# Optimization experiments

Hardware: AMD Instinct MI355X
Metric: run time of the kernel (lower is better)

Reference implementation:

```python
import jax, jax.numpy as jnp
import numpy as np
import math

B, S, D, H, W = 4, 8192, 1024, 16, 512  # batch, seq, d_model, heads, attention_window
HD = D // H


def setup_inputs() -> dict:
    key = jax.random.key(0)
    ks = jax.random.split(key, 5)
    scale = 0.02
    return {
        "x": jax.random.normal(ks[0], (B, S, D), dtype=jnp.float32),
        "wq": jax.random.normal(ks[1], (D, D), dtype=jnp.float32) * scale,
        "bq": jnp.zeros((D,), dtype=jnp.float32),
        "wk": jax.random.normal(ks[2], (D, D), dtype=jnp.float32) * scale,
        "bk": jnp.zeros((D,), dtype=jnp.float32),
        "wv": jax.random.normal(ks[3], (D, D), dtype=jnp.float32) * scale,
        "bv": jnp.zeros((D,), dtype=jnp.float32),
        "wo": jax.random.normal(ks[4], (D, D), dtype=jnp.float32) * scale,
        "bo": jnp.zeros((D,), dtype=jnp.float32),
    }


def reference(x, wq, bq, wk, bk, wv, bv, wo, bo):
    # torch Linear: y = x @ W.T + b
    q = (x @ wq.T + bq).reshape(B, S, H, HD)
    k = (x @ wk.T + bk).reshape(B, S, H, HD)
    v = (x @ wv.T + bv).reshape(B, S, H, HD)

    nb = S // W  # number of query blocks
    qb = q.reshape(B, nb, W, H, HD)

    # pad keys/values by W at the front so every block sees a 2W key window
    kp = jnp.pad(k, ((0, 0), (W, 0), (0, 0), (0, 0)))
    vp = jnp.pad(v, ((0, 0), (W, 0), (0, 0), (0, 0)))
    # padded key indices for block n: [n*W, n*W + 2W) <-> original [n*W - W, n*W + W)
    idx = jnp.arange(nb)[:, None] * W + jnp.arange(2 * W)[None, :]  # [nb, 2W]
    kb = kp[:, idx]  # [B, nb, 2W, H, HD]
    vb = vp[:, idx]  # [B, nb, 2W, H, HD]

    scores = jnp.einsum('bnqhd,bnkhd->bnhqk', qb, kb) / math.sqrt(HD)
    valid = (idx >= W)  # padded (out-of-range) keys only occur for block 0
    scores = jnp.where(valid[None, :, None, None, :], scores, -jnp.inf)
    attn = jax.nn.softmax(scores, axis=-1)  # softmax over the block's key window

    out = jnp.einsum('bnhqk,bnkhd->bnqhd', attn, vb).reshape(B, S, D)
    return out @ wo.T + bo
```

## Files before the change

kernel.cpp:

```cpp
#include <hip/hip_runtime.h>
#include <hip/hip_bf16.h>
#include <cstdint>

typedef __bf16 bf16;
typedef __attribute__((ext_vector_type(8))) __bf16 bf16x8;
typedef __attribute__((ext_vector_type(4))) __bf16 bf16x4;
typedef __attribute__((ext_vector_type(4))) float f32x4;
typedef __attribute__((ext_vector_type(4))) unsigned int u32x4;

#define B_ 4
#define S_ 8192
#define D_ 1024
#define H_ 16
#define HD_ 64
#define W_ 512
#define M_ (B_*S_)

#define EXP2F(x) __builtin_amdgcn_exp2f(x)
#define MFMA16(a,b,c) __builtin_amdgcn_mfma_f32_16x16x32_bf16(a,b,c,0,0,0)

__device__ __forceinline__ void async16(const void* g, void* l) {
  __builtin_amdgcn_global_load_lds(
      (const __attribute__((address_space(1))) unsigned int*)g,
      (__attribute__((address_space(3))) unsigned int*)l, 16, 0, 0);
}

__global__ void cast_f32_bf16(const float* __restrict__ in, bf16* __restrict__ out, int n4) {
  int i = blockIdx.x * blockDim.x + threadIdx.x;
  int stride = gridDim.x * blockDim.x;
  for (; i < n4; i += stride) {
    f32x4 v = ((const f32x4*)in)[i];
    bf16x4 o = { (bf16)v[0], (bf16)v[1], (bf16)v[2], (bf16)v[3] };
    ((bf16x4*)out)[i] = o;
  }
}

template<int MODE>
__global__ void __launch_bounds__(256, 2) gemm_bt(
    const bf16* __restrict__ A, const bf16* __restrict__ Bw,
    const float* __restrict__ bias, void* __restrict__ outp, float scale)
{
  constexpr int K = D_, N = D_;
  __shared__ bf16 As[128*32];
  __shared__ bf16 Bs[128*32];
  int bid = blockIdx.x;
  int nid = (bid & 7) * 256 + (bid >> 3);
  int bm = nid >> 3, bn = nid & 7;
  const int tid = threadIdx.x, lane = tid & 63;
  const int w = tid >> 6, wr = w >> 1, wc = w & 1;
  f32x4 acc[4][4] = {};
  const int r0 = tid >> 2;
  const int kbyte = (tid & 3) * 16;
  const char* Ab = (const char*)(A + (size_t)bm * 128 * K);
  const char* Bb = (const char*)(Bw + (size_t)bn * 128 * K);
  for (int kt = 0; kt < K; kt += 32) {
    __syncthreads();
    const size_t cb = (size_t)kt * 2 + kbyte;
    async16(Ab + (size_t)r0      * (K*2) + cb, (char*)As + tid*16);
    async16(Ab + (size_t)(r0+64) * (K*2) + cb, (char*)As + 4096 + tid*16);
    async16(Bb + (size_t)r0      * (K*2) + cb, (char*)Bs + tid*16);
    async16(Bb + (size_t)(r0+64) * (K*2) + cb, (char*)Bs + 4096 + tid*16);
    __syncthreads();
    bf16x8 a[4], b[4];
#pragma unroll
    for (int mi = 0; mi < 4; ++mi)
      a[mi] = *(const bf16x8*)(As + (wr*64 + mi*16 + (lane & 15))*32 + ((lane >> 4)*8));
#pragma unroll
    for (int ni = 0; ni < 4; ++ni)
      b[ni] = *(const bf16x8*)(Bs + (wc*64 + ni*16 + (lane & 15))*32 + ((lane >> 4)*8));
#pragma unroll
    for (int mi = 0; mi < 4; ++mi)
#pragma unroll
      for (int ni = 0; ni < 4; ++ni)
        acc[mi][ni] = MFMA16(a[mi], b[ni], acc[mi][ni]);
  }
  int row0 = bm*128 + wr*64, col0 = bn*128 + wc*64;
  int rsub = (lane >> 4) * 4;
#pragma unroll
  for (int ni = 0; ni < 4; ++ni) {
    int col = col0 + ni*16 + (lane & 15);
    float bz = bias[col];
#pragma unroll
    for (int mi = 0; mi < 4; ++mi) {
#pragma unroll
      for (int r = 0; r < 4; ++r) {
        int row = row0 + mi*16 + rsub + r;
        float v = (acc[mi][ni][r] + bz) * scale;
        if (MODE == 0) {
          ((bf16*)outp)[(size_t)row * N + col] = (bf16)v;
        } else if (MODE == 1) {
          ((bf16*)outp)[((size_t)(row >> 13) * D_ + col) * S_ + (row & (S_-1))] = (bf16)v;
        } else {
          ((float*)outp)[(size_t)row * N + col] = v;
        }
      }
    }
  }
}

__global__ void __launch_bounds__(256, 3) attn_kernel(
    const bf16* __restrict__ Q, const bf16* __restrict__ Kb,
    const bf16* __restrict__ Vt, bf16* __restrict__ Ao)
{
  __shared__ char Klds[2][8192];
  __shared__ char Vlds[2][8192];
  __shared__ char Plds[4][2048];
  int x = blockIdx.x;
  int xcd = x & 7, qt = (x >> 3) & 7, gg = x >> 6;
  int g = xcd + 8 * gg;
  int h = g & 15, n = (g >> 4) & 15, b = g >> 8;
  int tid = threadIdx.x, lane = tid & 63, w = tid >> 6;
  int g4 = lane >> 4, qi = lane & 15;
  int qrow = n * W_ + qt * 64 + w * 16;

  const size_t qoff = ((size_t)(b * S_ + qrow + qi)) * D_ + h * 64 + g4 * 8;
  bf16x8 qf0 = *(const bf16x8*)(Q + qoff);
  bf16x8 qf1 = *(const bf16x8*)(Q + qoff + 32);

  const bf16* Kg = Kb + ((size_t)b * S_) * D_ + h * 64;
  const bf16* Vg = Vt + ((size_t)(b * H_ + h) * HD_) * S_;

  const int srow = tid >> 3, scol = tid & 7;
  const int sswz = (srow & 7) << 4;

  f32x4 o[4] = {};
  float m_r = -3.0e38f, l_r = 0.f;
  const int fsw = (qi & 7) << 4;
  char* pb = &Plds[w][0];

  const int c0 = (n == 0) ? 8 : 0;
  const int ksbase = (n - 1) * W_;

  u32x4 pk0, pk1, pv0, pv1;
  {
    int ks = ksbase + c0 * 64;
    pk0 = *(const u32x4*)(Kg + (size_t)(ks + srow)      * D_ + scol * 8);
    pk1 = *(const u32x4*)(Kg + (size_t)(ks + srow + 32) * D_ + scol * 8);
    pv0 = *(const u32x4*)(Vg + (size_t)srow        * S_ + ks + scol * 8);
    pv1 = *(const u32x4*)(Vg + (size_t)(srow + 32) * S_ + ks + scol * 8);
    *(u32x4*)(Klds[0] + srow        * 128 + ((scol * 16) ^ sswz)) = pk0;
    *(u32x4*)(Klds[0] + (srow + 32) * 128 + ((scol * 16) ^ sswz)) = pk1;
    *(u32x4*)(Vlds[0] + srow        * 128 + ((scol * 16) ^ sswz)) = pv0;
    *(u32x4*)(Vlds[0] + (srow + 32) * 128 + ((scol * 16) ^ sswz)) = pv1;
  }
  __syncthreads();
  int cur = 0;
  for (int c = c0; c < 16; ++c) {
    bool pre = (c < 15);
    if (pre) {
      int ks2 = ksbase + (c + 1) * 64;
      pk0 = *(const u32x4*)(Kg + (size_t)(ks2 + srow)      * D_ + scol * 8);
      pk1 = *(const u32x4*)(Kg + (size_t)(ks2 + srow + 32) * D_ + scol * 8);
      pv0 = *(const u32x4*)(Vg + (size_t)srow        * S_ + ks2 + scol * 8);
      pv1 = *(const u32x4*)(Vg + (size_t)(srow + 32) * S_ + ks2 + scol * 8);
    }
    const char* kbuf = Klds[cur];
    const char* vbuf = Vlds[cur];
    f32x4 st[4];
    __builtin_amdgcn_s_setprio(1);
#pragma unroll
    for (int ni = 0; ni < 4; ++ni) {
      const char* kbase = kbuf + (ni * 16 + qi) * 128;
      bf16x8 kf0 = *(const bf16x8*)(kbase + ((g4 * 16) ^ fsw));
      bf16x8 kf1 = *(const bf16x8*)(kbase + ((64 + g4 * 16) ^ fsw));
      f32x4 z = {};
      z = MFMA16(kf0, qf0, z);
      z = MFMA16(kf1, qf1, z);
      st[ni] = z;
    }
    __builtin_amdgcn_s_setprio(0);
    float mx = st[0][0];
#pragma unroll
    for (int ni = 0; ni < 4; ++ni)
#pragma unroll
      for (int r = 0; r < 4; ++r) mx = fmaxf(mx, st[ni][r]);
    mx = fmaxf(mx, __shfl_xor(mx, 16));
    mx = fmaxf(mx, __shfl_xor(mx, 32));
    if (!__all(mx - m_r <= 8.0f)) {
      float mn = fmaxf(m_r, mx);
      float sc = EXP2F(m_r - mn);
      m_r = mn;
      l_r *= sc;
#pragma unroll
      for (int ai = 0; ai < 4; ++ai)
#pragma unroll
        for (int r = 0; r < 4; ++r) o[ai][r] *= sc;
    }
    float ls = 0.f;
    bf16x4 pw[4];
#pragma unroll
    for (int ni = 0; ni < 4; ++ni)
#pragma unroll
      for (int r = 0; r < 4; ++r) {
        float p = EXP2F(st[ni][r] - m_r);
        ls += p;
        pw[ni][r] = (bf16)p;
      }
    l_r += ls;
#pragma unroll
    for (int ni = 0; ni < 4; ++ni)
      *(bf16x4*)(pb + qi * 128 + ((ni * 32 + g4 * 8) ^ fsw)) = pw[ni];
    asm volatile("s_waitcnt lgkmcnt(0)" ::: "memory");
    __builtin_amdgcn_sched_barrier(0);
    bf16x8 pa0 = *(const bf16x8*)(pb + qi * 128 + ((g4 * 16) ^ fsw));
    bf16x8 pa1 = *(const bf16x8*)(pb + qi * 128 + ((64 + g4 * 16) ^ fsw));
    __builtin_amdgcn_sched_barrier(0x7F);
    __builtin_amdgcn_s_setprio(1);
#pragma unroll
    for (int ai = 0; ai < 4; ++ai) {
      const char* vbase = vbuf + (ai * 16 + qi) * 128;
      bf16x8 vf0 = *(const bf16x8*)(vbase + ((g4 * 16) ^ fsw));
      bf16x8 vf1 = *(const bf16x8*)(vbase + ((64 + g4 * 16) ^ fsw));
      o[ai] = MFMA16(vf0, pa0, o[ai]);
      o[ai] = MFMA16(vf1, pa1, o[ai]);
    }
    __builtin_amdgcn_s_setprio(0);
    if (pre) {
      int nb = cur ^ 1;
      *(u32x4*)(Klds[nb] + srow        * 128 + ((scol * 16) ^ sswz)) = pk0;
      *(u32x4*)(Klds[nb] + (srow + 32) * 128 + ((scol * 16) ^ sswz)) = pk1;
      *(u32x4*)(Vlds[nb] + srow        * 128 + ((scol * 16) ^ sswz)) = pv0;
      *(u32x4*)(Vlds[nb] + (srow + 32) * 128 + ((scol * 16) ^ sswz)) = pv1;
    }
    __syncthreads();
    cur ^= 1;
  }
  float lt = l_r + __shfl_xor(l_r, 16);
  lt += __shfl_xor(lt, 32);
  float inv = 1.0f / lt;
  size_t orow = ((size_t)(b * S_ + qrow + qi)) * D_ + h * 64 + g4 * 4;
#pragma unroll
  for (int ai = 0; ai < 4; ++ai) {
    bf16x4 ov;
#pragma unroll
    for (int r = 0; r < 4; ++r) ov[r] = (bf16)(o[ai][r] * inv);
    *(bf16x4*)(Ao + orow + ai * 16) = ov;
  }
}

extern "C" void kernel_launch(void* const* d_in, const int* in_sizes, int n_in,
                              void* d_out, int out_size, void* d_ws, size_t ws_size,
                              hipStream_t stream) {
  const float* x  = (const float*)d_in[0];
  const float* wq = (const float*)d_in[1];
  const float* bq = (const float*)d_in[2];
  const float* wk = (const float*)d_in[3];
  const float* bk = (const float*)d_in[4];
  const float* wv = (const float*)d_in[5];
  const float* bv = (const float*)d_in[6];
  const float* wo = (const float*)d_in[7];
  const float* bo = (const float*)d_in[8];
  float* out = (float*)d_out;

  char* ws = (char*)d_ws;
  const size_t sz = (size_t)M_ * D_ * 2;
  bf16* xb  = (bf16*)(ws + 0*sz);
  bf16* qb  = (bf16*)(ws + 1*sz);
  bf16* kb  = (bf16*)(ws + 2*sz);
  bf16* vt  = (bf16*)(ws + 3*sz);
  bf16* ao  = (bf16*)(ws + 4*sz);
  bf16* wqb = (bf16*)(ws + 5*sz);
  bf16* wkb = wqb + (size_t)D_*D_;
  bf16* wvb = wkb + (size_t)D_*D_;
  bf16* wob = wvb + (size_t)D_*D_;

  cast_f32_bf16<<<2048, 256, 0, stream>>>(x,  xb,  M_*D_/4);
  cast_f32_bf16<<<512,  256, 0, stream>>>(wq, wqb, D_*D_/4);
  cast_f32_bf16<<<512,  256, 0, stream>>>(wk, wkb, D_*D_/4);
  cast_f32_bf16<<<512,  256, 0, stream>>>(wv, wvb, D_*D_/4);
  cast_f32_bf16<<<512,  256, 0, stream>>>(wo, wob, D_*D_/4);

  gemm_bt<0><<<2048, 256, 0, stream>>>(xb, wqb, bq, qb, 0.125f * 1.44269504f);
  gemm_bt<0><<<2048, 256, 0, stream>>>(xb, wkb, bk, kb, 1.0f);
  gemm_bt<1><<<2048, 256, 0, stream>>>(xb, wvb, bv, vt, 1.0f);

  attn_kernel<<<8192, 256, 0, stream>>>(qb, kb, vt, ao);

  gemm_bt<2><<<2048, 256, 0, stream>>>(ao, wob, bo, out, 1.0f);
}
```

Baseline: 614.5 us.

## Use 32x32 MFMA register-resident P in attention and double-buffer GEMM LDS

The attention kernel moves from 16x16x32 to 32x32x16 MFMA tiles, with each wave handling 32 query rows, so the grid is halved. The P matrix is repacked in registers using cvt_pk_bf16 and permlane32_swap instead of a round-trip through LDS. Separately, the projection GEMM double-buffers its LDS tiles with async loads and explicit vmcnt waits so global loads overlap the MFMAs. The risks are higher register pressure in attention and correctness of the hand-written lane permutation and waitcnt sequencing.

```diff
diff --git a/kernel.cpp b/kernel.cpp
--- a/kernel.cpp
+++ b/kernel.cpp
@@ -6,6 +6,7 @@
 typedef __attribute__((ext_vector_type(8))) __bf16 bf16x8;
 typedef __attribute__((ext_vector_type(4))) __bf16 bf16x4;
 typedef __attribute__((ext_vector_type(4))) float f32x4;
+typedef __attribute__((ext_vector_type(16))) float f32x16;
 typedef __attribute__((ext_vector_type(4))) unsigned int u32x4;
 
 #define B_ 4
@@ -18,6 +19,7 @@
 
 #define EXP2F(x) __builtin_amdgcn_exp2f(x)
 #define MFMA16(a,b,c) __builtin_amdgcn_mfma_f32_16x16x32_bf16(a,b,c,0,0,0)
+#define MFMA32(a,b,c) __builtin_amdgcn_mfma_f32_32x32x16_bf16(a,b,c,0,0,0)
 
 __device__ __forceinline__ void async16(const void* g, void* l) {
   __builtin_amdgcn_global_load_lds(
@@ -41,8 +43,8 @@
     const float* __restrict__ bias, void* __restrict__ outp, float scale)
 {
   constexpr int K = D_, N = D_;
-  __shared__ bf16 As[128*32];
-  __shared__ bf16 Bs[128*32];
+  __shared__ bf16 As[2][128*32];
+  __shared__ bf16 Bs[2][128*32];
   int bid = blockIdx.x;
   int nid = (bid & 7) * 256 + (bid >> 3);
   int bm = nid >> 3, bn = nid & 7;
@@ -53,26 +55,38 @@
   const int kbyte = (tid & 3) * 16;
   const char* Ab = (const char*)(A + (size_t)bm * 128 * K);
   const char* Bb = (const char*)(Bw + (size_t)bn * 128 * K);
-  for (int kt = 0; kt < K; kt += 32) {
-    __syncthreads();
+
+  auto stage = [&](int kt, int buf) {
     const size_t cb = (size_t)kt * 2 + kbyte;
-    async16(Ab + (size_t)r0      * (K*2) + cb, (char*)As + tid*16);
-    async16(Ab + (size_t)(r0+64) * (K*2) + cb, (char*)As + 4096 + tid*16);
-    async16(Bb + (size_t)r0      * (K*2) + cb, (char*)Bs + tid*16);
-    async16(Bb + (size_t)(r0+64) * (K*2) + cb, (char*)Bs + 4096 + tid*16);
-    __syncthreads();
+    async16(Ab + (size_t)r0      * (K*2) + cb, (char*)&As[buf][0] + tid*16);
+    async16(Ab + (size_t)(r0+64) * (K*2) + cb, (char*)&As[buf][0] + 4096 + tid*16);
+    async16(Bb + (size_t)r0      * (K*2) + cb, (char*)&Bs[buf][0] + tid*16);
+    async16(Bb + (size_t)(r0+64) * (K*2) + cb, (char*)&Bs[buf][0] + 4096 + tid*16);
+  };
+
+  stage(0, 0);
+  for (int i = 0; i < 32; ++i) {
+    int cur = i & 1;
+    if (i < 31) {
+      stage((i + 1) * 32, cur ^ 1);
+      asm volatile("s_waitcnt vmcnt(4)" ::: "memory");
+    } else {
+      asm volatile("s_waitcnt vmcnt(0)" ::: "memory");
+    }
+    asm volatile("s_barrier" ::: "memory");
     bf16x8 a[4], b[4];
 #pragma unroll
     for (int mi = 0; mi < 4; ++mi)
-      a[mi] = *(const bf16x8*)(As + (wr*64 + mi*16 + (lane & 15))*32 + ((lane >> 4)*8));
+      a[mi] = *(const bf16x8*)(&As[cur][0] + (wr*64 + mi*16 + (lane & 15))*32 + ((lane >> 4)*8));
 #pragma unroll
     for (int ni = 0; ni < 4; ++ni)
-      b[ni] = *(const bf16x8*)(Bs + (wc*64 + ni*16 + (lane & 15))*32 + ((lane >> 4)*8));
+      b[ni] = *(const bf16x8*)(&Bs[cur][0] + (wc*64 + ni*16 + (lane & 15))*32 + ((lane >> 4)*8));
 #pragma unroll
     for (int mi = 0; mi < 4; ++mi)
 #pragma unroll
       for (int ni = 0; ni < 4; ++ni)
         acc[mi][ni] = MFMA16(a[mi], b[ni], acc[mi][ni]);
+    asm volatile("s_barrier" ::: "memory");
   }
   int row0 = bm*128 + wr*64, col0 = bn*128 + wc*64;
   int rsub = (lane >> 4) * 4;
@@ -104,29 +118,28 @@
 {
   __shared__ char Klds[2][8192];
   __shared__ char Vlds[2][8192];
-  __shared__ char Plds[4][2048];
   int x = blockIdx.x;
-  int xcd = x & 7, qt = (x >> 3) & 7, gg = x >> 6;
-  int g = xcd + 8 * gg;
+  int qt = (x >> 3) & 3;
+  int g  = (x & 7) + 8 * (x >> 5);
   int h = g & 15, n = (g >> 4) & 15, b = g >> 8;
   int tid = threadIdx.x, lane = tid & 63, w = tid >> 6;
-  int g4 = lane >> 4, qi = lane & 15;
-  int qrow = n * W_ + qt * 64 + w * 16;
-
-  const size_t qoff = ((size_t)(b * S_ + qrow + qi)) * D_ + h * 64 + g4 * 8;
-  bf16x8 qf0 = *(const bf16x8*)(Q + qoff);
-  bf16x8 qf1 = *(const bf16x8*)(Q + qoff + 32);
+  int hi = lane >> 5, qv = lane & 31;
+  int qrow = n * W_ + qt * 128 + w * 32;
+
+  const bf16* Qrow = Q + ((size_t)(b * S_ + qrow + qv)) * D_ + h * 64;
+  bf16x8 Qf[4];
+#pragma unroll
+  for (int s = 0; s < 4; ++s) Qf[s] = *(const bf16x8*)(Qrow + s * 16 + hi * 8);
 
   const bf16* Kg = Kb + ((size_t)b * S_) * D_ + h * 64;
   const bf16* Vg = Vt + ((size_t)(b * H_ + h) * HD_) * S_;
 
   const int srow = tid >> 3, scol = tid & 7;
   const int sswz = (srow & 7) << 4;
-
-  f32x4 o[4] = {};
+  const int fswq = (qv & 7) << 4;
+
+  f32x16 O0 = {}, O1 = {};
   float m_r = -3.0e38f, l_r = 0.f;
-  const int fsw = (qi & 7) << 4;
-  char* pb = &Plds[w][0];
 
   const int c0 = (n == 0) ? 8 : 0;
   const int ksbase = (n - 1) * W_;
@@ -156,25 +169,21 @@
     }
     const char* kbuf = Klds[cur];
     const char* vbuf = Vlds[cur];
-    f32x4 st[4];
+    f32x16 C0 = {}, C1 = {};
     __builtin_amdgcn_s_setprio(1);
 #pragma unroll
-    for (int ni = 0; ni < 4; ++ni) {
-      const char* kbase = kbuf + (ni * 16 + qi) * 128;
-      bf16x8 kf0 = *(const bf16x8*)(kbase + ((g4 * 16) ^ fsw));
-      bf16x8 kf1 = *(const bf16x8*)(kbase + ((64 + g4 * 16) ^ fsw));
-      f32x4 z = {};
-      z = MFMA16(kf0, qf0, z);
-      z = MFMA16(kf1, qf1, z);
-      st[ni] = z;
+    for (int s = 0; s < 4; ++s) {
+      bf16x8 k0 = *(const bf16x8*)(kbuf + qv * 128        + ((s * 32 + hi * 16) ^ fswq));
+      bf16x8 k1 = *(const bf16x8*)(kbuf + (32 + qv) * 128 + ((s * 32 + hi * 16) ^ fswq));
+      C0 = MFMA32(k0, Qf[s], C0);
+      C1 = MFMA32(k1, Qf[s], C1);
     }
     __builtin_amdgcn_s_setprio(0);
-    float mx = st[0][0];
-#pragma unroll
-    for (int ni = 0; ni < 4; ++ni)
-#pragma unroll
-      for (int r = 0; r < 4; ++r) mx = fmaxf(mx, st[ni][r]);
-    mx = fmaxf(mx, __shfl_xor(mx, 16));
+    float mx = C0[0];
+#pragma unroll
+    for (int r = 1; r < 16; ++r) mx = fmaxf(mx, C0[r]);
+#pragma unroll
+    for (int r = 0; r < 16; ++r) mx = fmaxf(mx, C1[r]);
     mx = fmaxf(mx, __shfl_xor(mx, 32));
     if (!__all(mx - m_r <= 8.0f)) {
       float mn = fmaxf(m_r, mx);
@@ -182,38 +191,48 @@
       m_r = mn;
       l_r *= sc;
 #pragma unroll
-      for (int ai = 0; ai < 4; ++ai)
-#pragma unroll
-        for (int r = 0; r < 4; ++r) o[ai][r] *= sc;
+      for (int r = 0; r < 16; ++r) { O0[r] *= sc; O1[r] *= sc; }
     }
     float ls = 0.f;
-    bf16x4 pw[4];
-#pragma unroll
-    for (int ni = 0; ni < 4; ++ni)
-#pragma unroll
-      for (int r = 0; r < 4; ++r) {
-        float p = EXP2F(st[ni][r] - m_r);
-        ls += p;
-        pw[ni][r] = (bf16)p;
+    float p0[16], p1[16];
+#pragma unroll
+    for (int r = 0; r < 16; ++r) {
+      p0[r] = EXP2F(C0[r] - m_r);
+      p1[r] = EXP2F(C1[r] - m_r);
+      ls += p0[r] + p1[r];
+    }
+    l_r += ls;
+    unsigned int L0[8], L1[8];
+#pragma unroll
+    for (int t = 0; t < 8; ++t) {
+      asm("v_cvt_pk_bf16_f32 %0, %1, %2" : "=v"(L0[t]) : "v"(p0[2*t]), "v"(p0[2*t+1]));
+      asm("v_cvt_pk_bf16_f32 %0, %1, %2" : "=v"(L1[t]) : "v"(p1[2*t]), "v"(p1[2*t+1]));
+    }
+    asm volatile("v_permlane32_swap_b32 %0, %1" : "+v"(L0[0]), "+v"(L0[2]));
+    asm volatile("v_permlane32_swap_b32 %0, %1" : "+v"(L0[1]), "+v"(L0[3]));
+    asm volatile("v_permlane32_swap_b32 %0, %1" : "+v"(L0[4]), "+v"(L0[6]));
+    asm volatile("v_permlane32_swap_b32 %0, %1" : "+v"(L0[5]), "+v"(L0[7]));
+    asm volatile("v_permlane32_swap_b32 %0, %1" : "+v"(L1[0]), "+v"(L1[2]));
+    asm volatile("v_permlane32_swap_b32 %0, %1" : "+v"(L1[1]), "+v"(L1[3]));
+    asm volatile("v_permlane32_swap_b32 %0, %1" : "+v"(L1[4]), "+v"(L1[6]));
+    asm volatile("v_permlane32_swap_b32 %0, %1" : "+v"(L1[5]), "+v"(L1[7]));
+    u32x4 F[2][2];
+    F[0][0] = u32x4{L0[0], L0[1], L0[2], L0[3]};
+    F[0][1] = u32x4{L0[4], L0[5], L0[6], L0[7]};
+    F[1][0] = u32x4{L1[0], L1[1], L1[2], L1[3]};
+    F[1][1] = u32x4{L1[4], L1[5], L1[6], L1[7]};
+    __builtin_amdgcn_s_setprio(1);
+#pragma unroll
+    for (int T = 0; T < 2; ++T)
+#pragma unroll
+      for (int s = 0; s < 2; ++s) {
+        bf16x8 pf = *(bf16x8*)&F[T][s];
+        int kbyteoff = T * 64 + s * 32 + hi * 16;
+        bf16x8 v0 = *(const bf16x8*)(vbuf + qv * 128        + (kbyteoff ^ fswq));
+        bf16x8 v1 = *(const bf16x8*)(vbuf + (32 + qv) * 128 + (kbyteoff ^ fswq));
+        O0 = MFMA32(v0, pf, O0);
+        O1 = MFMA32(v1, pf, O1);
       }
-    l_r += ls;
-#pragma unroll
-    for (int ni = 0; ni < 4; ++ni)
-      *(bf16x4*)(pb + qi * 128 + ((ni * 32 + g4 * 8) ^ fsw)) = pw[ni];
-    asm volatile("s_waitcnt lgkmcnt(0)" ::: "memory");
-    __builtin_amdgcn_sched_barrier(0);
-    bf16x8 pa0 = *(const bf16x8*)(pb + qi * 128 + ((g4 * 16) ^ fsw));
-    bf16x8 pa1 = *(const bf16x8*)(pb + qi * 128 + ((64 + g4 * 16) ^ fsw));
-    __builtin_amdgcn_sched_barrier(0x7F);
-    __builtin_amdgcn_s_setprio(1);
-#pragma unroll
-    for (int ai = 0; ai < 4; ++ai) {
-      const char* vbase = vbuf + (ai * 16 + qi) * 128;
-      bf16x8 vf0 = *(const bf16x8*)(vbase + ((g4 * 16) ^ fsw));
-      bf16x8 vf1 = *(const bf16x8*)(vbase + ((64 + g4 * 16) ^ fsw));
-      o[ai] = MFMA16(vf0, pa0, o[ai]);
-      o[ai] = MFMA16(vf1, pa1, o[ai]);
-    }
     __builtin_amdgcn_s_setprio(0);
     if (pre) {
       int nb = cur ^ 1;
@@ -225,16 +244,22 @@
     __syncthreads();
     cur ^= 1;
   }
-  float lt = l_r + __shfl_xor(l_r, 16);
-  lt += __shfl_xor(lt, 32);
+  float lt = l_r + __shfl_xor(l_r, 32);
   float inv = 1.0f / lt;
-  size_t orow = ((size_t)(b * S_ + qrow + qi)) * D_ + h * 64 + g4 * 4;
-#pragma unroll
-  for (int ai = 0; ai < 4; ++ai) {
-    bf16x4 ov;
-#pragma unroll
-    for (int r = 0; r < 4; ++r) ov[r] = (bf16)(o[ai][r] * inv);
-    *(bf16x4*)(Ao + orow + ai * 16) = ov;
+  size_t obase = ((size_t)(b * S_ + qrow + qv)) * D_ + h * 64;
+#pragma unroll
+  for (int ot = 0; ot < 2; ++ot) {
+#pragma unroll
+    for (int rq = 0; rq < 4; ++rq) {
+      int hd = ot * 32 + 8 * rq + 4 * hi;
+      bf16x4 ov;
+#pragma unroll
+      for (int j = 0; j < 4; ++j) {
+        float val = (ot == 0 ? O0[rq*4 + j] : O1[rq*4 + j]) * inv;
+        ov[j] = (bf16)val;
+      }
+      *(bf16x4*)(Ao + obase + hd) = ov;
+    }
   }
 }
 
@@ -274,7 +299,7 @@
   gemm_bt<0><<<2048, 256, 0, stream>>>(xb, wkb, bk, kb, 1.0f);
   gemm_bt<1><<<2048, 256, 0, stream>>>(xb, wvb, bv, vt, 1.0f);
 
-  attn_kernel<<<8192, 256, 0, stream>>>(qb, kb, vt, ao);
+  attn_kernel<<<4096, 256, 0, stream>>>(qb, kb, vt, ao);
 
   gemm_bt<2><<<2048, 256, 0, stream>>>(ao, wob, bo, out, 1.0f);
 }
```

Measured after the change: 575.5 us. -6.4%, faster.
